# Kernel tuning notes

Measured on AMD Instinct MI355X. Metric: run time of the kernel, lower is better.

The kernel has to match this reference:

```python
import jax, jax.numpy as jnp
import numpy as np

EPS = 1e-08
BASE_CR = 0.5
MIN_CR = 0.1


def _layernorm(h, g, b, eps=1e-5):
    m = jnp.mean(h, axis=-1, keepdims=True)
    v = jnp.mean((h - m) ** 2, axis=-1, keepdims=True)
    return (h - m) * jax.lax.rsqrt(v + eps) * g + b


def _normalize(h, eps=1e-12):
    n = jnp.sqrt(jnp.sum(h * h, axis=-1, keepdims=True))
    return h / jnp.maximum(n, eps)


def _conv1d(h, w, b):
    # h: [B,S,D], w: [K,I,O] (WIO), cross-correlation, SAME padding (torch Conv1d padding=1, k=3)
    y = jax.lax.conv_general_dilated(h, w, window_strides=(1,), padding='SAME',
                                     dimension_numbers=('NWC', 'WIO', 'NWC'))
    return y + b


def setup_inputs() -> dict:
    key = jax.random.key(0)
    ks = jax.random.split(key, 8)
    V, L, D, B, S = 50257, 2048, 1024, 8, 2048
    inp = {
        'x': jax.random.randint(ks[0], (B, S), 0, V),
        'token_emb': jax.random.normal(ks[1], (V, D), jnp.float32) * 0.02,
        'pos_emb': jax.random.normal(ks[2], (L, D), jnp.float32) * 0.02,
        'conv1_w': jax.random.normal(ks[3], (3, D, D), jnp.float32) * 0.025,
        'conv1_b': jnp.zeros((D,), jnp.float32),
        'conv2_w': jax.random.normal(ks[4], (3, D, D), jnp.float32) * 0.025,
        'conv2_b': jnp.zeros((D,), jnp.float32),
        'proj_w': jax.random.normal(ks[5], (D, D), jnp.float32) * 0.03,
        'proj_b': jnp.zeros((D,), jnp.float32),
        'ph_w': jax.random.normal(ks[6], (D, D), jnp.float32) * 0.03,
        'ph_b': jnp.zeros((D,), jnp.float32),
        'ln_g': jnp.ones((D,), jnp.float32),
        'ln_b': jnp.zeros((D,), jnp.float32),
    }
    return inp


def reference(x, token_emb, pos_emb, conv1_w, conv1_b, conv2_w, conv2_b,
              proj_w, proj_b, ph_w, ph_b, ln_g, ln_b):
    B, S = x.shape
    # token + position embedding
    h = token_emb[x] + pos_emb[:S][None, :, :]                 # [B,S,D]
    # two conv1d + gelu (exact erf, matching torch F.gelu default)
    h = jax.nn.gelu(_conv1d(h, conv1_w, conv1_b), approximate=False)
    h = jax.nn.gelu(_conv1d(h, conv2_w, conv2_b), approximate=False)
    h = _layernorm(h, ln_g, ln_b)
    # dropout is identity in eval mode
    # S is a power of two -> next_power_of_two(S) == S, no padding
    x_fft = jnp.fft.fft(h, axis=1)                              # [B,S,D] complex64
    magnitude = jnp.abs(x_fft)
    thresh = 0.1 * jnp.max(magnitude, axis=1, keepdims=True)
    complexity = jnp.mean((magnitude > thresh).astype(jnp.float32), axis=(1, 2))  # [B]
    cr = jnp.clip(BASE_CR * (1.0 - complexity), MIN_CR, 1.0)
    N = jnp.clip((cr * S).astype(jnp.int32), 1, S)              # [B] kept coefficients
    # vectorized ragged masking (replaces per-sample python loop/scatter)
    mask = (jnp.arange(S)[None, :] < N[:, None]).astype(jnp.float32)   # [B,S]
    x_fft_c = x_fft * mask[:, :, None]
    x_ifft_raw = jnp.fft.ifft(x_fft_c, n=S, axis=1).real        # [B,S,D]
    proj_out = x_ifft_raw @ proj_w + proj_b
    x_ifft = _layernorm(proj_out, ln_g, ln_b)
    recon_target = proj_out                                     # same proj of same ifft
    # loss
    cos_sim = jnp.sum(_normalize(x_ifft) * _normalize(recon_target), axis=-1)
    cos_sim = jnp.clip(cos_sim, -1.0 + EPS, 1.0 - EPS)
    d = x_ifft - recon_target
    l1 = jnp.where(jnp.abs(d) < 1.0, 0.5 * d * d, jnp.abs(d) - 0.5)    # smooth_l1, beta=1
    proj_x = x_ifft @ ph_w + ph_b
    proj_t = recon_target @ ph_w + ph_b
    sem = jnp.mean((_normalize(proj_x) - _normalize(proj_t)) ** 2, axis=-1)  # [B,S]
    combined = 0.6 * jnp.mean(1.0 - cos_sim) + 0.2 * jnp.mean(l1, axis=-1) + 0.2 * sem
    loss = jnp.sum(combined * mask) / (jnp.sum(mask) + EPS)
    return (x_ifft, loss)
```

## Files before the change

### kernel.cpp

```cpp
#include <hip/hip_runtime.h>
#include <math.h>

#define S_LEN 2048
#define D_DIM 1024
#define B_BATCH 8
#define R_ROWS (B_BATCH * S_LEN)
#define BD_ROWS (B_BATCH * D_DIM)
#define PAD_ROWS 2050

typedef unsigned short u16;
typedef unsigned int u32;
typedef __attribute__((ext_vector_type(8))) short bf16x8;
typedef __attribute__((ext_vector_type(4))) float f32x4;

__device__ __forceinline__ u16 f2bf(float f) {
    u32 x = __float_as_uint(f);
    u32 r = (x + 0x7fffu + ((x >> 16) & 1u)) >> 16;
    return (u16)r;
}
__device__ __forceinline__ float bf2f(u16 u) {
    return __uint_as_float(((u32)u) << 16);
}
__device__ __forceinline__ float gelu_exact(float x) {
    return 0.5f * x * (1.0f + erff(x * 0.70710678118654752f));
}
__device__ __forceinline__ int dr4(int v) {
    v = __brev((unsigned)v) >> 22;
    return ((v & 0x155) << 1) | ((v >> 1) & 0x155);
}
#define PIDX(i) ((i) + ((i) >> 5))

#define GLDS(gsrc, ldst)                                                                   \
    __builtin_amdgcn_global_load_lds(                                                      \
        (const __attribute__((address_space(1))) u32*)(gsrc),                              \
        (__attribute__((address_space(3))) u32*)(ldst), 16, 0, 0)

#define WAIT_LGKM0 do { asm volatile("s_waitcnt lgkmcnt(0)" ::: "memory");                 \
                        __builtin_amdgcn_sched_barrier(0); } while (0)
#define WAIT_VM(n)   do { asm volatile("s_waitcnt vmcnt(" #n ")" ::: "memory");            \
                          __builtin_amdgcn_sched_barrier(0); } while (0)

__global__ __launch_bounds__(256) void zero_pads(u16* __restrict__ P0, u16* __restrict__ P1)
{
    const int bid = blockIdx.x;
    u16* P = (bid >= 16) ? P1 : P0;
    const int ridx = bid & 15;
    const int b = ridx >> 1;
    const size_t row = (size_t)b * PAD_ROWS + (size_t)(ridx & 1) * (PAD_ROWS - 1);
    ((uint2*)(P + row * D_DIM))[threadIdx.x] = make_uint2(0u, 0u);
}

__global__ __launch_bounds__(256) void wconv(const float* __restrict__ W, u16* __restrict__ WT)
{
    __shared__ float t[32][33];
    const int tap = blockIdx.z;
    const int n0 = blockIdx.x * 32, k0 = blockIdx.y * 32;
    const int tx = threadIdx.x, ty = threadIdx.y;
    const float* ip = W + (size_t)tap * D_DIM * D_DIM;
    u16* op = WT + (size_t)tap * D_DIM * D_DIM;
#pragma unroll
    for (int u = 0; u < 4; u++)
        t[ty + u * 8][tx] = ip[(size_t)(k0 + ty + u * 8) * D_DIM + n0 + tx];
    __syncthreads();
#pragma unroll
    for (int u = 0; u < 4; u++)
        op[(size_t)(n0 + ty + u * 8) * D_DIM + k0 + tx] = f2bf(t[tx][ty + u * 8]);
}

__global__ __launch_bounds__(256) void wconv_inter(
    const float* __restrict__ W, const float* __restrict__ g, u16* __restrict__ WTI)
{
    __shared__ float t[32][33];
    const int n0 = blockIdx.x * 32, k0 = blockIdx.y * 32;
    const int tx = threadIdx.x, ty = threadIdx.y;
#pragma unroll
    for (int u = 0; u < 4; u++)
        t[ty + u * 8][tx] = W[(size_t)(k0 + ty + u * 8) * D_DIM + n0 + tx];
    __syncthreads();
    const float gk = g[k0 + tx];
#pragma unroll
    for (int u = 0; u < 4; u++) {
        const int n = n0 + ty + u * 8;
        const float w = t[tx][ty + u * 8];
        WTI[((size_t)(2 * n) << 10) + k0 + tx] = f2bf(w);
        WTI[((size_t)(2 * n + 1) << 10) + k0 + tx] = f2bf(w * gk);
    }
}

__global__ __launch_bounds__(256) void gemv_ph(
    const u16* __restrict__ WTI, const float* __restrict__ lnb,
    const float* __restrict__ phb, float* __restrict__ vg, float* __restrict__ c0)
{
    const int wid = threadIdx.x >> 6, lane = threadIdx.x & 63;
    const int n = blockIdx.x * 4 + wid;
    const u16* r0 = WTI + ((size_t)(2 * n) << 10) + lane * 16;
    const u16* r1 = WTI + ((size_t)(2 * n + 1) << 10) + lane * 16;
    float sb = 0.f, sg = 0.f;
#pragma unroll
    for (int h = 0; h < 2; h++) {
        uint4 w0 = *(const uint4*)(r0 + h * 8);
        uint4 w1 = *(const uint4*)(r1 + h * 8);
        float a[8], b8[8];
        a[0] = bf2f((u16)(w0.x & 0xffff)); a[1] = bf2f((u16)(w0.x >> 16));
        a[2] = bf2f((u16)(w0.y & 0xffff)); a[3] = bf2f((u16)(w0.y >> 16));
        a[4] = bf2f((u16)(w0.z & 0xffff)); a[5] = bf2f((u16)(w0.z >> 16));
        a[6] = bf2f((u16)(w0.w & 0xffff)); a[7] = bf2f((u16)(w0.w >> 16));
        b8[0] = bf2f((u16)(w1.x & 0xffff)); b8[1] = bf2f((u16)(w1.x >> 16));
        b8[2] = bf2f((u16)(w1.y & 0xffff)); b8[3] = bf2f((u16)(w1.y >> 16));
        b8[4] = bf2f((u16)(w1.z & 0xffff)); b8[5] = bf2f((u16)(w1.z >> 16));
        b8[6] = bf2f((u16)(w1.w & 0xffff)); b8[7] = bf2f((u16)(w1.w >> 16));
        const int kb = lane * 16 + h * 8;
        float4 l0 = *(const float4*)(lnb + kb), l1 = *(const float4*)(lnb + kb + 4);
        sb += a[0]*l0.x + a[1]*l0.y + a[2]*l0.z + a[3]*l0.w
            + a[4]*l1.x + a[5]*l1.y + a[6]*l1.z + a[7]*l1.w;
        sg += b8[0] + b8[1] + b8[2] + b8[3] + b8[4] + b8[5] + b8[6] + b8[7];
    }
#pragma unroll
    for (int off = 32; off > 0; off >>= 1) {
        sg += __shfl_xor(sg, off);
        sb += __shfl_xor(sb, off);
    }
    if (lane == 0) { vg[n] = sg; c0[n] = sb + phb[n]; }
}

__global__ __launch_bounds__(256) void emb_kernel(
    const int* __restrict__ x, const float* __restrict__ tok,
    const float* __restrict__ pos, u16* __restrict__ P0)
{
    const int row = blockIdx.x;
    const int tid = threadIdx.x;
    const int t = x[row];
    const int s = row & (S_LEN - 1);
    const int b = row >> 11;
    float4 a = ((const float4*)(tok + (size_t)t * D_DIM))[tid];
    float4 p = ((const float4*)(pos + (size_t)s * D_DIM))[tid];
    uint2 v;
    v.x = (u32)f2bf(a.x + p.x) | ((u32)f2bf(a.y + p.y) << 16);
    v.y = (u32)f2bf(a.z + p.z) | ((u32)f2bf(a.w + p.w) << 16);
    ((uint2*)(P0 + ((size_t)b * PAD_ROWS + 1 + s) * D_DIM))[tid] = v;
}

__global__ __launch_bounds__(512, 2) void gemm_8ph(
    const u16* __restrict__ A, const u16* __restrict__ WT,
    const float* __restrict__ bias,
    float* __restrict__ outF, u16* __restrict__ outB,
    float* __restrict__ rowS, float* __restrict__ rowQ,
    int ntaps, int doGelu, int aPadded, int outBPadded)
{
    __shared__ u16 As[2][2][8192];
    __shared__ u16 Bs[2][2][8192];
    const int tid = threadIdx.x;
    const int wid = tid >> 6, lane = tid & 63;
    const int wm = wid >> 2, wn = wid & 3;
    const int l15 = lane & 15, l4 = lane >> 4;
    const int flat = blockIdx.y * 4 + blockIdx.x;
    const int xcd = flat & 7;
    const int ii = flat >> 3;
    const int by = xcd * 8 + (ii >> 2);
    const int bx = ii & 3;
    const int row0 = by * 256;
    const int col0 = bx * 256;
    const int b = row0 >> 11;
    const int srow0 = row0 & (S_LEN - 1);
    const int nt = ntaps * 16;
    const int NI = nt >> 1;

    const int stR = tid >> 2;
    const int stKc = (((tid & 3) ^ ((tid >> 3) & 3)) << 3);
    const int ldsOff = tid * 16;
    const int swz4 = ((l4 ^ ((l15 >> 1) & 3)) << 4);

#define STAGE_A(T_, s_) do {                                                               \
        const int tap_ = (T_) >> 4;                                                        \
        const int kb_ = ((T_) & 15) * 64 + (s_) * 32 + stKc;                               \
        const size_t ar_ = (aPadded ? (size_t)(b * PAD_ROWS + srow0 + tap_)                \
                                    : (size_t)row0);                                       \
        GLDS(A + ((ar_ + stR) << 10) + kb_,                                                \
             (char*)&As[(T_) & 1][s_][0] + ldsOff);                                        \
        GLDS(A + ((ar_ + stR + 128) << 10) + kb_,                                          \
             (char*)&As[(T_) & 1][s_][0] + ldsOff + 8192);                                 \
    } while (0)
#define STAGE_B(T_, s_) do {                                                               \
        const int tap_ = (T_) >> 4;                                                        \
        const int kb_ = ((T_) & 15) * 64 + (s_) * 32 + stKc;                               \
        const u16* wp_ = WT + ((size_t)tap_ << 20) + ((size_t)(col0 + stR) << 10) + kb_;   \
        GLDS(wp_, (char*)&Bs[(T_) & 1][s_][0] + ldsOff);                                   \
        GLDS(wp_ + (size_t)(128 << 10), (char*)&Bs[(T_) & 1][s_][0] + ldsOff + 8192);      \
    } while (0)
#define RD_A(dst_, buf_, s_, mih_) do {                                                    \
        const char* p_ = (const char*)&As[buf_][s_][0]                                     \
                         + (size_t)(wm * 128 + (mih_) * 64 + l15) * 64 + swz4;             \
        dst_[0] = *(const bf16x8*)(p_);                                                    \
        dst_[1] = *(const bf16x8*)(p_ + 1024);                                             \
        dst_[2] = *(const bf16x8*)(p_ + 2048);                                             \
        dst_[3] = *(const bf16x8*)(p_ + 3072);                                             \
    } while (0)
#define RD_B(dst_, buf_, s_) do {                                                          \
        const char* p_ = (const char*)&Bs[buf_][s_][0]                                     \
                         + (size_t)(wn * 64 + l15) * 64 + swz4;                            \
        dst_[0] = *(const bf16x8*)(p_);                                                    \
        dst_[1] = *(const bf16x8*)(p_ + 1024);                                             \
        dst_[2] = *(const bf16x8*)(p_ + 2048);                                             \
        dst_[3] = *(const bf16x8*)(p_ + 3072);                                             \
    } while (0)
#define MF(mih_, av_, bv_) do {                                                            \
        __builtin_amdgcn_s_setprio(1);                                                     \
        _Pragma("unroll")                                                                  \
        for (int mi_ = 0; mi_ < 4; mi_++)                                                  \
            _Pragma("unroll")                                                              \
            for (int ni_ = 0; ni_ < 4; ni_++)                                              \
                acc[(mih_) * 4 + mi_][ni_] = __builtin_amdgcn_mfma_f32_16x16x32_bf16(      \
                    av_[mi_], bv_[ni_], acc[(mih_) * 4 + mi_][ni_], 0, 0, 0);              \
        __builtin_amdgcn_s_setprio(0);                                                     \
    } while (0)
#define BAR __builtin_amdgcn_s_barrier()

    f32x4 acc[8][4];
#pragma unroll
    for (int m = 0; m < 8; m++)
#pragma unroll
        for (int n = 0; n < 4; n++) acc[m][n] = (f32x4){0.f, 0.f, 0.f, 0.f};

    STAGE_A(0, 0); STAGE_B(0, 0);
    STAGE_A(0, 1); STAGE_B(0, 1);
    STAGE_A(1, 0); STAGE_B(1, 0);
    WAIT_VM(4);
    BAR;

    for (int i = 0; i < NI; ++i) {
        const int o = 2 * i + 1;
        const int e2 = 2 * i + 2, o2 = 2 * i + 3;
        const bool last = (i == NI - 1);
        bf16x8 a[4], bv[4];
        RD_A(a, 0, 0, 0); RD_B(bv, 0, 0);
        STAGE_A(o, 1);
        BAR; WAIT_LGKM0;
        MF(0, a, bv);
        BAR;
        RD_A(a, 0, 0, 1);
        STAGE_B(o, 1);
        BAR; WAIT_LGKM0;
        MF(1, a, bv);
        BAR;
        RD_A(a, 0, 1, 0); RD_B(bv, 0, 1);
        if (!last) STAGE_A(e2, 0);
        BAR; WAIT_LGKM0;
        MF(0, a, bv);
        BAR;
        RD_A(a, 0, 1, 1);
        if (!last) STAGE_B(e2, 0);
        BAR; WAIT_LGKM0;
        MF(1, a, bv);
        if (last) { WAIT_VM(0); } else { WAIT_VM(4); }
        BAR;
        RD_A(a, 1, 0, 0); RD_B(bv, 1, 0);
        if (!last) STAGE_A(e2, 1);
        BAR; WAIT_LGKM0;
        MF(0, a, bv);
        BAR;
        RD_A(a, 1, 0, 1);
        if (!last) STAGE_B(e2, 1);
        BAR; WAIT_LGKM0;
        MF(1, a, bv);
        BAR;
        RD_A(a, 1, 1, 0); RD_B(bv, 1, 1);
        if (!last) STAGE_A(o2, 0);
        BAR; WAIT_LGKM0;
        MF(0, a, bv);
        BAR;
        RD_A(a, 1, 1, 1);
        if (!last) STAGE_B(o2, 0);
        BAR; WAIT_LGKM0;
        MF(1, a, bv);
        if (!last) { WAIT_VM(4); }
        BAR;
    }
#undef STAGE_A

    float bb[4];
#pragma unroll
    for (int ni = 0; ni < 4; ni++) bb[ni] = bias[col0 + wn * 64 + ni * 16 + l15];

#pragma unroll
    for (int mi = 0; mi < 8; mi++) {
#pragma unroll
        for (int reg = 0; reg < 4; reg++) {
            const int row = row0 + wm * 128 + mi * 16 + l4 * 4 + reg;
            float s_ = 0.f, q_ = 0.f;
#pragma unroll
            for (int ni = 0; ni < 4; ni++) {
                const int col = col0 + wn * 64 + ni * 16 + l15;
                float v = acc[mi][ni][reg] + bb[ni];
                if (doGelu) v = gelu_exact(v);
                if (outF) outF[(size_t)row * D_DIM + col] = v;
                if (outB) {
                    const size_t orow = outBPadded
                        ? ((size_t)(row >> 11) * PAD_ROWS + 1 + (size_t)(row & (S_LEN - 1)))
                        : (size_t)row;
                    outB[orow * D_DIM + col] = f2bf(v);
                }
                if (rowS) { s_ += v; q_ = fmaf(v, v, q_); }
            }
            if (rowS) {
#pragma unroll
                for (int off = 1; off < 16; off <<= 1) {
                    s_ += __shfl_xor(s_, off);
                    q_ += __shfl_xor(q_, off);
                }
                if (l15 == 0) {
                    atomicAdd(&rowS[row], s_);
                    atomicAdd(&rowQ[row], q_);
                }
            }
        }
    }
}

__global__ __launch_bounds__(512, 2) void phstats_8ph(
    const u16* __restrict__ A, const u16* __restrict__ WTI,
    const float* __restrict__ phb, const float* __restrict__ vg,
    const float* __restrict__ c0,
    const float* __restrict__ rowS2, const float* __restrict__ rowQ2,
    const int* __restrict__ Ndev,
    float* __restrict__ Sxx, float* __restrict__ Stt, float* __restrict__ Sxt)
{
    __shared__ u16 As[2][2][8192];
    __shared__ u16 Bs[2][2][8192];
    const int tid = threadIdx.x;
    const int wid = tid >> 6, lane = tid & 63;
    const int wm = wid >> 2, wn = wid & 3;
    const int l15 = lane & 15, l4 = lane >> 4;
    const int flat = blockIdx.y * 8 + blockIdx.x;
    const int xcd = flat & 7;
    const int ii = flat >> 3;
    const int by = xcd * 4 + (ii >> 3);
    const int bx = ii & 7;
    const int batch = by >> 2;
    const int rb = by & 3;
    if (rb * 256 >= Ndev[batch]) return;
    const int row0 = batch * S_LEN + rb * 256;
    const int col0 = bx * 256;
    const int NI = 8;

    const int stR = tid >> 2;
    const int stKc = (((tid & 3) ^ ((tid >> 3) & 3)) << 3);
    const int ldsOff = tid * 16;
    const int swz4 = ((l4 ^ ((l15 >> 1) & 3)) << 4);

#define STAGE_A(T_, s_) do {                                                               \
        const int kb_ = ((T_) & 15) * 64 + (s_) * 32 + stKc;                               \
        GLDS(A + (((size_t)row0 + stR) << 10) + kb_,                                       \
             (char*)&As[(T_) & 1][s_][0] + ldsOff);                                        \
        GLDS(A + (((size_t)row0 + stR + 128) << 10) + kb_,                                 \
             (char*)&As[(T_) & 1][s_][0] + ldsOff + 8192);                                 \
    } while (0)
#define STAGE_BI(T_, s_) do {                                                              \
        const int kb_ = ((T_) & 15) * 64 + (s_) * 32 + stKc;                               \
        const u16* wp_ = WTI + ((size_t)(col0 + stR) << 10) + kb_;                         \
        GLDS(wp_, (char*)&Bs[(T_) & 1][s_][0] + ldsOff);                                   \
        GLDS(wp_ + (size_t)(128 << 10), (char*)&Bs[(T_) & 1][s_][0] + ldsOff + 8192);      \
    } while (0)

    f32x4 acc[8][4];
#pragma unroll
    for (int m = 0; m < 8; m++)
#pragma unroll
        for (int n = 0; n < 4; n++) acc[m][n] = (f32x4){0.f, 0.f, 0.f, 0.f};

    STAGE_A(0, 0); STAGE_BI(0, 0);
    STAGE_A(0, 1); STAGE_BI(0, 1);
    STAGE_A(1, 0); STAGE_BI(1, 0);
    WAIT_VM(4);
    BAR;

    for (int i = 0; i < NI; ++i) {
        const int o = 2 * i + 1;
        const int e2 = 2 * i + 2, o2 = 2 * i + 3;
        const bool last = (i == NI - 1);
        bf16x8 a[4], bv[4];
        RD_A(a, 0, 0, 0); RD_B(bv, 0, 0);
        STAGE_A(o, 1);
        BAR; WAIT_LGKM0;
        MF(0, a, bv);
        BAR;
        RD_A(a, 0, 0, 1);
        STAGE_BI(o, 1);
        BAR; WAIT_LGKM0;
        MF(1, a, bv);
        BAR;
        RD_A(a, 0, 1, 0); RD_B(bv, 0, 1);
        if (!last) STAGE_A(e2, 0);
        BAR; WAIT_LGKM0;
        MF(0, a, bv);
        BAR;
        RD_A(a, 0, 1, 1);
        if (!last) STAGE_BI(e2, 0);
        BAR; WAIT_LGKM0;
        MF(1, a, bv);
        if (last) { WAIT_VM(0); } else { WAIT_VM(4); }
        BAR;
        RD_A(a, 1, 0, 0); RD_B(bv, 1, 0);
        if (!last) STAGE_A(e2, 1);
        BAR; WAIT_LGKM0;
        MF(0, a, bv);
        BAR;
        RD_A(a, 1, 0, 1);
        if (!last) STAGE_BI(e2, 1);
        BAR; WAIT_LGKM0;
        MF(1, a, bv);
        BAR;
        RD_A(a, 1, 1, 0); RD_B(bv, 1, 1);
        if (!last) STAGE_A(o2, 0);
        BAR; WAIT_LGKM0;
        MF(0, a, bv);
        BAR;
        RD_A(a, 1, 1, 1);
        if (!last) STAGE_BI(o2, 0);
        BAR; WAIT_LGKM0;
        MF(1, a, bv);
        if (!last) { WAIT_VM(4); }
        BAR;
    }
#undef STAGE_A
#undef STAGE_BI
#undef RD_A
#undef RD_B
#undef MF
#undef BAR

    float phv[4], vgv[4], c0v[4];
#pragma unroll
    for (int ni = 0; ni < 4; ni++) {
        const int col = col0 + wn * 64 + ni * 16 + l15;
        const int j = col >> 1;
        phv[ni] = phb[j]; vgv[ni] = vg[j]; c0v[ni] = c0[j];
    }
    const bool odd = (l15 & 1) != 0;
#pragma unroll
    for (int mi = 0; mi < 8; mi++) {
#pragma unroll
        for (int reg = 0; reg < 4; reg++) {
            const int row = row0 + wm * 128 + mi * 16 + l4 * 4 + reg;
            const float mS = rowS2[row] * (1.0f / D_DIM);
            const float var = rowQ2[row] * (1.0f / D_DIM) - mS * mS;
            const float rsv = rsqrtf(var + 1e-5f);
            const float mrs = mS * rsv;
            float sxx = 0.f, stt = 0.f, sxt = 0.f;
#pragma unroll
            for (int ni = 0; ni < 4; ni++) {
                const float raw = acc[mi][ni][reg];
                const float val = odd ? (rsv * raw - mrs * vgv[ni] + c0v[ni])
                                      : (raw + phv[ni]);
                const float par = __shfl_xor(val, 1);
                const float pt = odd ? par : val;
                const float px = odd ? val : par;
                stt = fmaf(pt, pt, stt);
                sxx = fmaf(px, px, sxx);
                sxt = fmaf(pt, px, sxt);
            }
#pragma unroll
            for (int off = 1; off < 16; off <<= 1) {
                sxx += __shfl_xor(sxx, off);
                stt += __shfl_xor(stt, off);
                sxt += __shfl_xor(sxt, off);
            }
            if (l15 == 0) {
                atomicAdd(&Sxx[row], 0.5f * sxx);
                atomicAdd(&Stt[row], 0.5f * stt);
                atomicAdd(&Sxt[row], 0.5f * sxt);
            }
        }
    }
}

__global__ __launch_bounds__(256) void transposeLN(
    const u16* __restrict__ in, const float* __restrict__ rowS,
    const float* __restrict__ rowQ,
    const float* __restrict__ g, const float* __restrict__ beta,
    float* __restrict__ out)
{
    __shared__ float t[32][33];
    const int b = blockIdx.z;
    const int n0 = blockIdx.x * 32, m0 = blockIdx.y * 32;
    const int tx = threadIdx.x, ty = threadIdx.y;
    const u16* ip = in + (size_t)b * S_LEN * D_DIM;
    float* op = out + (size_t)b * S_LEN * D_DIM;
#pragma unroll
    for (int u = 0; u < 4; u++)
        t[ty + u * 8][tx] = bf2f(ip[(size_t)(m0 + ty + u * 8) * D_DIM + n0 + tx]);
    __syncthreads();
    const int row = b * S_LEN + m0 + tx;
    const float mS = rowS[row] * (1.0f / D_DIM);
    const float var = rowQ[row] * (1.0f / D_DIM) - mS * mS;
    const float rs = rsqrtf(var + 1e-5f);
#pragma unroll
    for (int u = 0; u < 4; u++) {
        const int d = n0 + ty + u * 8;
        const float val = (t[tx][ty + u * 8] - mS) * rs * g[d] + beta[d];
        op[(size_t)d * S_LEN + m0 + tx] = val;
    }
}

__global__ __launch_bounds__(256) void fft_fwd(
    const float* __restrict__ in, u32* __restrict__ X, int* __restrict__ counts)
{
    __shared__ float re[1056], im[1056], twr[1024], twi[1024];
    __shared__ float redf[4];
    __shared__ int redi[4];
    const int tid = threadIdx.x;
    const int row = blockIdx.x;
    const float2* src = (const float2*)(in + (size_t)row * S_LEN);
#pragma unroll
    for (int u = 0; u < 4; u++) {
        int e = tid + u * 256;
        float ang = -3.14159265358979f * (float)e * (1.0f / 512.0f);
        float sn, cs; __sincosf(ang, &sn, &cs);
        twr[e] = cs; twi[e] = sn;
    }
#pragma unroll
    for (int u = 0; u < 4; u++) {
        int t = tid + u * 256;
        float2 z = src[t];
        int p = PIDX(dr4(t));
        re[p] = z.x; im[p] = z.y;
    }
    __syncthreads();
#pragma unroll
    for (int s = 1; s <= 5; ++s) {
        const int mq = 1 << (2 * (s - 1));
        const int fsh = 2 * (5 - s);
        const int j = tid & (mq - 1);
        const int g = tid >> (2 * (s - 1));
        const int i0 = (g << (2 * s)) + j;
        const int e1 = j << fsh;
        const int p0 = PIDX(i0), p1 = PIDX(i0 + mq), p2 = PIDX(i0 + 2 * mq), p3 = PIDX(i0 + 3 * mq);
        float a0r = re[p0], a0i = im[p0];
        float a1r = re[p1], a1i = im[p1];
        float a2r = re[p2], a2i = im[p2];
        float a3r = re[p3], a3i = im[p3];
        float w1r = twr[e1], w1i = twi[e1];
        float w2r = twr[2 * e1], w2i = twi[2 * e1];
        float w3r = twr[3 * e1], w3i = twi[3 * e1];
        float b1r = a1r * w1r - a1i * w1i, b1i = a1r * w1i + a1i * w1r;
        float b2r = a2r * w2r - a2i * w2i, b2i = a2r * w2i + a2i * w2r;
        float b3r = a3r * w3r - a3i * w3i, b3i = a3r * w3i + a3i * w3r;
        float t0r = a0r + b2r, t0i = a0i + b2i;
        float t1r = a0r - b2r, t1i = a0i - b2i;
        float t2r = b1r + b3r, t2i = b1i + b3i;
        float t3r = b1r - b3r, t3i = b1i - b3i;
        re[p0] = t0r + t2r; im[p0] = t0i + t2i;
        re[p2] = t0r - t2r; im[p2] = t0i - t2i;
        re[p1] = t1r + t3i; im[p1] = t1i - t3r;
        re[p3] = t1r - t3i; im[p3] = t1i + t3r;
        __syncthreads();
    }
    u32* dst = X + (size_t)row * 1024;
    float mag[4];
    float xtra = 0.0f;
    float lmax = 0.0f;
#pragma unroll
    for (int u = 0; u < 4; u++) {
        int k = tid + u * 256;
        int mk = (1024 - k) & 1023;
        float rk = re[PIDX(k)], ik = im[PIDX(k)];
        float rm = re[PIDX(mk)], imm = im[PIDX(mk)];
        float er = 0.5f * (rk + rm);
        float ei = 0.5f * (ik - imm);
        float orr = 0.5f * (ik + imm);
        float oii = -0.5f * (rk - rm);
        float ang = -3.14159265358979f * (float)k * (1.0f / 1024.0f);
        float sn, cs; __sincosf(ang, &sn, &cs);
        float xr = er + orr * cs - oii * sn;
        float xi = ei + orr * sn + oii * cs;
        dst[k] = (u32)f2bf(xr) | ((u32)f2bf(xi) << 16);
        float m2 = xr * xr + xi * xi;
        mag[u] = m2;
        lmax = fmaxf(lmax, m2);
        if (k == 0) {
            float x1024 = re[PIDX(0)] - im[PIDX(0)];
            xtra = x1024 * x1024;
            lmax = fmaxf(lmax, xtra);
        }
    }
#pragma unroll
    for (int off = 32; off > 0; off >>= 1) lmax = fmaxf(lmax, __shfl_xor(lmax, off));
    if ((tid & 63) == 0) redf[tid >> 6] = lmax;
    __syncthreads();
    const float bmax = fmaxf(fmaxf(redf[0], redf[1]), fmaxf(redf[2], redf[3]));
    const float thr = 0.01f * bmax;
    int lc = 0;
#pragma unroll
    for (int u = 0; u < 4; u++) {
        int k = tid + u * 256;
        lc += (mag[u] > thr) ? ((k == 0) ? 1 : 2) : 0;
    }
    if (tid == 0) lc += (xtra > thr) ? 1 : 0;
#pragma unroll
    for (int off = 32; off > 0; off >>= 1) lc += __shfl_xor(lc, off);
    if ((tid & 63) == 0) redi[tid >> 6] = lc;
    __syncthreads();
    if (tid == 0)
        atomicAdd(&counts[(row >> 10) * 64 + (row & 63)],
                  redi[0] + redi[1] + redi[2] + redi[3]);
}

__global__ void calc_n(const int* __restrict__ counts, int* __restrict__ Ndev)
{
// ... 191 lines not shown
        rowA[row] = 1.0f - cs;
        rowL1[row] = l1;
    }
}

__global__ __launch_bounds__(1024) void final_loss(
    const float* __restrict__ rowA, const float* __restrict__ rowL1,
    const float* __restrict__ Sxx, const float* __restrict__ Stt,
    const float* __restrict__ Sxt,
    const int* __restrict__ Ndev, float* __restrict__ out)
{
    const int tid = threadIdx.x;
    float sa = 0.f, sb = 0.f;
#pragma unroll
    for (int i = 0; i < 16; i++) {
        int r = tid + i * 1024;
        sa += rowA[r];
        int b = r >> 11, s = r & (S_LEN - 1);
        if (s < Ndev[b]) {
            float sx = Sxx[r], st = Stt[r], sxtv = Sxt[r];
            float nxx = fmaxf(sqrtf(sx), 1e-12f);
            float ntt = fmaxf(sqrtf(st), 1e-12f);
            float sem = (sx / (nxx * nxx) + st / (ntt * ntt)
                         - 2.0f * sxtv / (nxx * ntt)) * (1.0f / D_DIM);
            sb += 0.2f * (rowL1[r] * (1.0f / D_DIM)) + 0.2f * sem;
        }
    }
#pragma unroll
    for (int off = 32; off > 0; off >>= 1) {
        sa += __shfl_xor(sa, off);
        sb += __shfl_xor(sb, off);
    }
    __shared__ float ra[16], rb[16];
    if ((tid & 63) == 0) { ra[tid >> 6] = sa; rb[tid >> 6] = sb; }
    __syncthreads();
    if (tid == 0) {
        float A = 0.f, Bs = 0.f;
#pragma unroll
        for (int i = 0; i < 16; i++) { A += ra[i]; Bs += rb[i]; }
        int K = 0;
        for (int b = 0; b < B_BATCH; b++) K += Ndev[b];
        float Kf = (float)K;
        float M = A * (1.0f / 16384.0f);
        out[(size_t)R_ROWS * D_DIM] = (0.6f * M * Kf + Bs) / (Kf + 1e-8f);
    }
}

extern "C" void kernel_launch(void* const* d_in, const int* in_sizes, int n_in,
                              void* d_out, int out_size, void* d_ws, size_t ws_size,
                              hipStream_t stream)
{
    (void)in_sizes; (void)n_in; (void)out_size; (void)ws_size;
    const int*   x       = (const int*)  d_in[0];
    const float* tok     = (const float*)d_in[1];
    const float* pos     = (const float*)d_in[2];
    const float* conv1_w = (const float*)d_in[3];
    const float* conv1_b = (const float*)d_in[4];
    const float* conv2_w = (const float*)d_in[5];
    const float* conv2_b = (const float*)d_in[6];
    const float* proj_w  = (const float*)d_in[7];
    const float* proj_b  = (const float*)d_in[8];
    const float* ph_w    = (const float*)d_in[9];
    const float* ph_b    = (const float*)d_in[10];
    const float* ln_g    = (const float*)d_in[11];
    const float* ln_b    = (const float*)d_in[12];
    float* out = (float*)d_out;

    char* ws = (char*)d_ws;
    int*    counts = (int*)(ws);
    int*    Ndev   = (int*)(ws + 2048);
    float*  Sxx    = (float*)(ws + 266240);
    float*  Stt    = (float*)(ws + 331776);
    float*  Sxt    = (float*)(ws + 397312);
    float*  rowA   = (float*)(ws + 462848);
    float*  rowL1  = (float*)(ws + 528384);
    float*  vg     = (float*)(ws + 593920);
    float*  c0     = (float*)(ws + 598016);
    float*  rowS   = (float*)(ws + 602112);
    float*  rowQ   = (float*)(ws + 667648);
    float*  rowS2  = (float*)(ws + 733184);
    float*  rowQ2  = (float*)(ws + 798720);
    const size_t MB = 1ull << 20;
    u16*   WT   = (u16*)(ws + 1 * MB);
    u16*   WTI  = WT;
    u16*   P0   = (u16*)(ws + 17 * MB);
    u16*   P1   = (u16*)(ws + 50 * MB);
    u32*   Xs   = (u32*)(ws + 83 * MB);
    float* F32B = (float*)(ws + 148 * MB);

    hipMemsetAsync(ws, 0, MB, stream);
    zero_pads<<<32, 256, 0, stream>>>(P0, P1);
    wconv<<<dim3(32, 32, 3), dim3(32, 8), 0, stream>>>(conv1_w, WT);
    wconv<<<dim3(32, 32, 3), dim3(32, 8), 0, stream>>>(conv2_w, WT + 3u * (1u << 20));
    wconv<<<dim3(32, 32, 1), dim3(32, 8), 0, stream>>>(proj_w, WT + 6u * (1u << 20));
    emb_kernel<<<R_ROWS, 256, 0, stream>>>(x, tok, pos, P0);
    gemm_8ph<<<dim3(4, 64), 512, 0, stream>>>(P0, WT, conv1_b,
                                              nullptr, P1, nullptr, nullptr, 3, 1, 1, 1);
    wconv_inter<<<dim3(32, 32, 1), dim3(32, 8), 0, stream>>>(ph_w, ln_g, WTI);
    gemv_ph<<<256, 256, 0, stream>>>(WTI, ln_b, ph_b, vg, c0);
    gemm_8ph<<<dim3(4, 64), 512, 0, stream>>>(P1, WT + 3u * (1u << 20), conv2_b,
                                              nullptr, P0, rowS, rowQ, 3, 1, 1, 0);
    transposeLN<<<dim3(32, 64, 8), dim3(32, 8), 0, stream>>>(P0, rowS, rowQ,
                                                             ln_g, ln_b, F32B);
    fft_fwd<<<BD_ROWS, 256, 0, stream>>>(F32B, Xs, counts);
    calc_n<<<1, 64, 0, stream>>>(counts, Ndev);
    fft_inv<<<BD_ROWS, 256, 0, stream>>>(Xs, Ndev, P1);
    transpose_bb<<<dim3(64, 32, 8), dim3(32, 8), 0, stream>>>(P1, P0, D_DIM, S_LEN);
    gemm_8ph<<<dim3(4, 64), 512, 0, stream>>>(P0, WT + 6u * (1u << 20), proj_b,
                                              nullptr, P1, rowS2, rowQ2, 1, 0, 0, 0);
    ln_loss<<<R_ROWS, 256, 0, stream>>>(P1, ln_g, ln_b, out, rowS2, rowQ2, rowA, rowL1);
    phstats_8ph<<<dim3(8, 32), 512, 0, stream>>>(P1, WTI, ph_b, vg, c0,
                                                 rowS2, rowQ2, Ndev, Sxx, Stt, Sxt);
    final_loss<<<1, 1024, 0, stream>>>(rowA, rowL1, Sxx, Stt, Sxt, Ndev, out);
}
```

Baseline: 537.3 us.

## Add dedicated conv GEMM kernel, merge weight prep, store LN transpose as bf16

The two conv layers now run in a new gemm_c2 kernel. It uses 256x128 tiles, a three-buffer LDS pipeline and four blocks per CU, in place of the generic 256x256 gemm_8ph with two blocks per CU. The four weight-conversion launches are merged into one wprep kernel, and the ph GEMV is moved earlier. The transposed LayerNorm output feeding the FFT is stored as packed bf16 instead of fp32, which halves that intermediate's traffic. The bf16 FFT input costs some precision, and the smaller conv tiles reload the A operand more often.

```diff
diff --git a/kernel.cpp b/kernel.cpp
--- a/kernel.cpp
+++ b/kernel.cpp
@@ -50,40 +50,39 @@
     ((uint2*)(P + row * D_DIM))[threadIdx.x] = make_uint2(0u, 0u);
 }
 
-__global__ __launch_bounds__(256) void wconv(const float* __restrict__ W, u16* __restrict__ WT)
+__global__ __launch_bounds__(256) void wprep(
+    const float* __restrict__ c1, const float* __restrict__ c2,
+    const float* __restrict__ pj, const float* __restrict__ ph,
+    const float* __restrict__ g, u16* __restrict__ WT)
 {
     __shared__ float t[32][33];
-    const int tap = blockIdx.z;
+    const int z = blockIdx.z;
     const int n0 = blockIdx.x * 32, k0 = blockIdx.y * 32;
     const int tx = threadIdx.x, ty = threadIdx.y;
-    const float* ip = W + (size_t)tap * D_DIM * D_DIM;
-    u16* op = WT + (size_t)tap * D_DIM * D_DIM;
+    const float* src;
+    if (z < 3)      src = c1 + (size_t)z * D_DIM * D_DIM;
+    else if (z < 6) src = c2 + (size_t)(z - 3) * D_DIM * D_DIM;
+    else if (z == 6) src = pj;
+    else            src = ph;
 #pragma unroll
     for (int u = 0; u < 4; u++)
-        t[ty + u * 8][tx] = ip[(size_t)(k0 + ty + u * 8) * D_DIM + n0 + tx];
+        t[ty + u * 8][tx] = src[(size_t)(k0 + ty + u * 8) * D_DIM + n0 + tx];
     __syncthreads();
-#pragma unroll
-    for (int u = 0; u < 4; u++)
-        op[(size_t)(n0 + ty + u * 8) * D_DIM + k0 + tx] = f2bf(t[tx][ty + u * 8]);
-}
-
-__global__ __launch_bounds__(256) void wconv_inter(
-    const float* __restrict__ W, const float* __restrict__ g, u16* __restrict__ WTI)
-{
-    __shared__ float t[32][33];
-    const int n0 = blockIdx.x * 32, k0 = blockIdx.y * 32;
-    const int tx = threadIdx.x, ty = threadIdx.y;
-#pragma unroll
-    for (int u = 0; u < 4; u++)
-        t[ty + u * 8][tx] = W[(size_t)(k0 + ty + u * 8) * D_DIM + n0 + tx];
-    __syncthreads();
-    const float gk = g[k0 + tx];
-#pragma unroll
-    for (int u = 0; u < 4; u++) {
-        const int n = n0 + ty + u * 8;
-        const float w = t[tx][ty + u * 8];
-        WTI[((size_t)(2 * n) << 10) + k0 + tx] = f2bf(w);
-        WTI[((size_t)(2 * n + 1) << 10) + k0 + tx] = f2bf(w * gk);
+    if (z < 7) {
+        u16* op = WT + (size_t)z * D_DIM * D_DIM;
+#pragma unroll
+        for (int u = 0; u < 4; u++)
+            op[(size_t)(n0 + ty + u * 8) * D_DIM + k0 + tx] = f2bf(t[tx][ty + u * 8]);
+    } else {
+        u16* WTI = WT + 7u * (1u << 20);
+        const float gk = g[k0 + tx];
+#pragma unroll
+        for (int u = 0; u < 4; u++) {
+            const int n = n0 + ty + u * 8;
+            const float w = t[tx][ty + u * 8];
+            WTI[((size_t)(2 * n) << 10) + k0 + tx] = f2bf(w);
+            WTI[((size_t)(2 * n + 1) << 10) + k0 + tx] = f2bf(w * gk);
+        }
     }
 }
 
@@ -140,12 +139,146 @@
     ((uint2*)(P0 + ((size_t)b * PAD_ROWS + 1 + s) * D_DIM))[tid] = v;
 }
 
+__global__ __launch_bounds__(512, 4) void gemm_c2(
+    const u16* __restrict__ A, const u16* __restrict__ WT,
+    const float* __restrict__ bias, u16* __restrict__ outB,
+    float* __restrict__ rowS, float* __restrict__ rowQ,
+    int outBPadded)
+{
+    __shared__ u16 As[3][8192];
+    __shared__ u16 Bs[3][4096];
+    const int tid = threadIdx.x;
+    const int wid = tid >> 6, lane = tid & 63;
+    const int wm = wid >> 1, wn = wid & 1;
+    const int l15 = lane & 15, l4 = lane >> 4;
+    const int flat = blockIdx.y * 8 + blockIdx.x;
+    const int xcd = flat & 7;
+    const int ii = flat >> 3;
+    const int by = xcd * 8 + (ii >> 3);
+    const int bx = ii & 7;
+    const int row0 = by * 256;
+    const int col0 = bx * 128;
+    const int b = row0 >> 11;
+    const int srow0 = row0 & (S_LEN - 1);
+    const int nt = 96;
+
+    const int stR = tid >> 2;
+    const int stKc = (((tid & 3) ^ ((tid >> 3) & 3)) << 3);
+    const int ldsOff = tid * 16;
+    const int swz4 = ((l4 ^ ((l15 >> 1) & 3)) << 4);
+
+#define C2_SA(T_, B_) do {                                                                 \
+        const int tap_ = (T_) >> 5;                                                        \
+        const int kb_ = ((T_) & 31) * 32 + stKc;                                           \
+        const size_t ar_ = (size_t)(b * PAD_ROWS + srow0 + tap_);                          \
+        GLDS(A + ((ar_ + stR) << 10) + kb_, (char*)&As[B_][0] + ldsOff);                   \
+        GLDS(A + ((ar_ + stR + 128) << 10) + kb_, (char*)&As[B_][0] + ldsOff + 8192);      \
+    } while (0)
+#define C2_SB(T_, B_) do {                                                                 \
+        const int tap_ = (T_) >> 5;                                                        \
+        const int kb_ = ((T_) & 31) * 32 + stKc;                                           \
+        GLDS(WT + ((size_t)tap_ << 20) + ((size_t)(col0 + stR) << 10) + kb_,               \
+             (char*)&Bs[B_][0] + ldsOff);                                                  \
+    } while (0)
+#define C2_RA(B_) do {                                                                     \
+        const char* p_ = (const char*)&As[B_][0] + (size_t)(wm * 64 + l15) * 64 + swz4;    \
+        a[0] = *(const bf16x8*)(p_);                                                       \
+        a[1] = *(const bf16x8*)(p_ + 1024);                                                \
+        a[2] = *(const bf16x8*)(p_ + 2048);                                                \
+        a[3] = *(const bf16x8*)(p_ + 3072);                                                \
+    } while (0)
+#define C2_RB(B_) do {                                                                     \
+        const char* p_ = (const char*)&Bs[B_][0] + (size_t)(wn * 64 + l15) * 64 + swz4;    \
+        bv[0] = *(const bf16x8*)(p_);                                                      \
+        bv[1] = *(const bf16x8*)(p_ + 1024);                                               \
+        bv[2] = *(const bf16x8*)(p_ + 2048);                                               \
+        bv[3] = *(const bf16x8*)(p_ + 3072);                                               \
+    } while (0)
+#define C2_MF do {                                                                         \
+        __builtin_amdgcn_s_setprio(1);                                                     \
+        _Pragma("unroll")                                                                  \
+        for (int mi_ = 0; mi_ < 4; mi_++)                                                  \
+            _Pragma("unroll")                                                              \
+            for (int ni_ = 0; ni_ < 4; ni_++)                                              \
+                acc[mi_][ni_] = __builtin_amdgcn_mfma_f32_16x16x32_bf16(                   \
+                    a[mi_], bv[ni_], acc[mi_][ni_], 0, 0, 0);                              \
+        __builtin_amdgcn_s_setprio(0);                                                     \
+    } while (0)
+#define C2_BAR __builtin_amdgcn_s_barrier()
+#define C2_SUB(TT_, RB_, SB_) do {                                                         \
+        C2_RA(RB_); C2_RB(RB_);                                                            \
+        if ((TT_) + 2 < nt) { C2_SA((TT_) + 2, SB_); C2_SB((TT_) + 2, SB_); }              \
+        C2_BAR; WAIT_LGKM0;                                                                \
+        C2_MF;                                                                             \
+        if ((TT_) + 2 < nt) { WAIT_VM(3); } else { WAIT_VM(0); }                           \
+        C2_BAR;                                                                            \
+    } while (0)
+
+    f32x4 acc[4][4];
+#pragma unroll
+    for (int m = 0; m < 4; m++)
+#pragma unroll
+        for (int n = 0; n < 4; n++) acc[m][n] = (f32x4){0.f, 0.f, 0.f, 0.f};
+
+    bf16x8 a[4], bv[4];
+    C2_SA(0, 0); C2_SB(0, 0);
+    C2_SA(1, 1); C2_SB(1, 1);
+    WAIT_VM(3);
+    C2_BAR;
+
+    for (int t = 0; t < nt; t += 3) {
+        C2_SUB(t,     0, 2);
+        C2_SUB(t + 1, 1, 0);
+        C2_SUB(t + 2, 2, 1);
+    }
+#undef C2_SA
+#undef C2_SB
+#undef C2_RA
+#undef C2_RB
+#undef C2_MF
+#undef C2_BAR
+#undef C2_SUB
+
+    float bb[4];
+#pragma unroll
+    for (int ni = 0; ni < 4; ni++) bb[ni] = bias[col0 + wn * 64 + ni * 16 + l15];
+
+#pragma unroll
+    for (int mi = 0; mi < 4; mi++) {
+#pragma unroll
+        for (int reg = 0; reg < 4; reg++) {
+            const int row = row0 + wm * 64 + mi * 16 + l4 * 4 + reg;
+            float s_ = 0.f, q_ = 0.f;
+#pragma unroll
+            for (int ni = 0; ni < 4; ni++) {
+                const int col = col0 + wn * 64 + ni * 16 + l15;
+                float v = gelu_exact(acc[mi][ni][reg] + bb[ni]);
+                const size_t orow = outBPadded
+                    ? ((size_t)(row >> 11) * PAD_ROWS + 1 + (size_t)(row & (S_LEN - 1)))
+                    : (size_t)row;
+                outB[orow * D_DIM + col] = f2bf(v);
+                if (rowS) { s_ += v; q_ = fmaf(v, v, q_); }
+            }
+            if (rowS) {
+#pragma unroll
+                for (int off = 1; off < 16; off <<= 1) {
+                    s_ += __shfl_xor(s_, off);
+                    q_ += __shfl_xor(q_, off);
+                }
+                if (l15 == 0) {
+                    atomicAdd(&rowS[row], s_);
+                    atomicAdd(&rowQ[row], q_);
+                }
+            }
+        }
+    }
+}
+
 __global__ __launch_bounds__(512, 2) void gemm_8ph(
     const u16* __restrict__ A, const u16* __restrict__ WT,
     const float* __restrict__ bias,
-    float* __restrict__ outF, u16* __restrict__ outB,
-    float* __restrict__ rowS, float* __restrict__ rowQ,
-    int ntaps, int doGelu, int aPadded, int outBPadded)
+    u16* __restrict__ outB,
+    float* __restrict__ rowS, float* __restrict__ rowQ)
 {
     __shared__ u16 As[2][2][8192];
     __shared__ u16 Bs[2][2][8192];
@@ -160,10 +293,7 @@
     const int bx = ii & 3;
     const int row0 = by * 256;
     const int col0 = bx * 256;
-    const int b = row0 >> 11;
-    const int srow0 = row0 & (S_LEN - 1);
-    const int nt = ntaps * 16;
-    const int NI = nt >> 1;
+    const int NI = 8;
 
     const int stR = tid >> 2;
     const int stKc = (((tid & 3) ^ ((tid >> 3) & 3)) << 3);
@@ -171,19 +301,15 @@
     const int swz4 = ((l4 ^ ((l15 >> 1) & 3)) << 4);
 
 #define STAGE_A(T_, s_) do {                                                               \
-        const int tap_ = (T_) >> 4;                                                        \
         const int kb_ = ((T_) & 15) * 64 + (s_) * 32 + stKc;                               \
-        const size_t ar_ = (aPadded ? (size_t)(b * PAD_ROWS + srow0 + tap_)                \
-                                    : (size_t)row0);                                       \
-        GLDS(A + ((ar_ + stR) << 10) + kb_,                                                \
+        GLDS(A + (((size_t)row0 + stR) << 10) + kb_,                                       \
              (char*)&As[(T_) & 1][s_][0] + ldsOff);                                        \
-        GLDS(A + ((ar_ + stR + 128) << 10) + kb_,                                          \
+        GLDS(A + (((size_t)row0 + stR + 128) << 10) + kb_,                                 \
              (char*)&As[(T_) & 1][s_][0] + ldsOff + 8192);                                 \
     } while (0)
 #define STAGE_B(T_, s_) do {                                                               \
-        const int tap_ = (T_) >> 4;                                                        \
         const int kb_ = ((T_) & 15) * 64 + (s_) * 32 + stKc;                               \
-        const u16* wp_ = WT + ((size_t)tap_ << 20) + ((size_t)(col0 + stR) << 10) + kb_;   \
+        const u16* wp_ = WT + ((size_t)(col0 + stR) << 10) + kb_;                          \
         GLDS(wp_, (char*)&Bs[(T_) & 1][s_][0] + ldsOff);                                   \
         GLDS(wp_ + (size_t)(128 << 10), (char*)&Bs[(T_) & 1][s_][0] + ldsOff + 8192);      \
     } while (0)
@@ -214,6 +340,55 @@
         __builtin_amdgcn_s_setprio(0);                                                     \
     } while (0)
 #define BAR __builtin_amdgcn_s_barrier()
+#define LOOP8PH                                                                            \
+    for (int i = 0; i < NI; ++i) {                                                         \
+        const int o = 2 * i + 1;                                                           \
+        const int e2 = 2 * i + 2, o2 = 2 * i + 3;                                          \
+        const bool last = (i == NI - 1);                                                   \
+        bf16x8 a[4], bv[4];                                                                \
+        RD_A(a, 0, 0, 0); RD_B(bv, 0, 0);                                                  \
+        STAGE_A(o, 1);                                                                     \
+        BAR; WAIT_LGKM0;                                                                   \
+        MF(0, a, bv);                                                                      \
+        BAR;                                                                               \
+        RD_A(a, 0, 0, 1);                                                                  \
+        STAGE_B(o, 1);                                                                     \
+        BAR; WAIT_LGKM0;                                                                   \
+        MF(1, a, bv);                                                                      \
+        BAR;                                                                               \
+        RD_A(a, 0, 1, 0); RD_B(bv, 0, 1);                                                  \
+        if (!last) STAGE_A(e2, 0);                                                         \
+        BAR; WAIT_LGKM0;                                                                   \
+        MF(0, a, bv);                                                                      \
+        BAR;                                                                               \
+        RD_A(a, 0, 1, 1);                                                                  \
+        if (!last) STAGE_B(e2, 0);                                                         \
+        BAR; WAIT_LGKM0;                                                                   \
+        MF(1, a, bv);                                                                      \
+        if (last) { WAIT_VM(0); } else { WAIT_VM(4); }                                     \
+        BAR;                                                                               \
+        RD_A(a, 1, 0, 0); RD_B(bv, 1, 0);                                                  \
+        if (!last) STAGE_A(e2, 1);                                                         \
+        BAR; WAIT_LGKM0;                                                                   \
+        MF(0, a, bv);                                                                      \
+        BAR;                                                                               \
+        RD_A(a, 1, 0, 1);                                                                  \
+        if (!last) STAGE_B(e2, 1);                                                         \
+        BAR; WAIT_LGKM0;                                                                   \
+        MF(1, a, bv);                                                                      \
+        BAR;                                                                               \
+        RD_A(a, 1, 1, 0); RD_B(bv, 1, 1);                                                  \
+        if (!last) STAGE_A(o2, 0);                                                         \
+        BAR; WAIT_LGKM0;                                                                   \
+        MF(0, a, bv);                                                                      \
+        BAR;                                                                               \
+        RD_A(a, 1, 1, 1);                                                                  \
+        if (!last) STAGE_B(o2, 0);                                                         \
+        BAR; WAIT_LGKM0;                                                                   \
+        MF(1, a, bv);                                                                      \
+        if (!last) { WAIT_VM(4); }                                                         \
+        BAR;                                                                               \
+    }
 
     f32x4 acc[8][4];
 #pragma unroll
@@ -226,56 +401,7 @@
     STAGE_A(1, 0); STAGE_B(1, 0);
     WAIT_VM(4);
     BAR;
-
-    for (int i = 0; i < NI; ++i) {
-        const int o = 2 * i + 1;
-        const int e2 = 2 * i + 2, o2 = 2 * i + 3;
-        const bool last = (i == NI - 1);
-        bf16x8 a[4], bv[4];
-        RD_A(a, 0, 0, 0); RD_B(bv, 0, 0);
-        STAGE_A(o, 1);
-        BAR; WAIT_LGKM0;
-        MF(0, a, bv);
-        BAR;
-        RD_A(a, 0, 0, 1);
-        STAGE_B(o, 1);
-        BAR; WAIT_LGKM0;
-        MF(1, a, bv);
-        BAR;
-        RD_A(a, 0, 1, 0); RD_B(bv, 0, 1);
-        if (!last) STAGE_A(e2, 0);
-        BAR; WAIT_LGKM0;
-        MF(0, a, bv);
-        BAR;
-        RD_A(a, 0, 1, 1);
-        if (!last) STAGE_B(e2, 0);
-        BAR; WAIT_LGKM0;
-        MF(1, a, bv);
-        if (last) { WAIT_VM(0); } else { WAIT_VM(4); }
-        BAR;
-        RD_A(a, 1, 0, 0); RD_B(bv, 1, 0);
-        if (!last) STAGE_A(e2, 1);
-        BAR; WAIT_LGKM0;
-        MF(0, a, bv);
-        BAR;
-        RD_A(a, 1, 0, 1);
-        if (!last) STAGE_B(e2, 1);
-        BAR; WAIT_LGKM0;
-        MF(1, a, bv);
-        BAR;
-        RD_A(a, 1, 1, 0); RD_B(bv, 1, 1);
-        if (!last) STAGE_A(o2, 0);
-        BAR; WAIT_LGKM0;
-        MF(0, a, bv);
-        BAR;
-        RD_A(a, 1, 1, 1);
-        if (!last) STAGE_B(o2, 0);
-        BAR; WAIT_LGKM0;
-        MF(1, a, bv);
-        if (!last) { WAIT_VM(4); }
-        BAR;
-    }
-#undef STAGE_A
+    LOOP8PH
 
     float bb[4];
 #pragma unroll
@@ -291,33 +417,24 @@
             for (int ni = 0; ni < 4; ni++) {
                 const int col = col0 + wn * 64 + ni * 16 + l15;
                 float v = acc[mi][ni][reg] + bb[ni];
-                if (doGelu) v = gelu_exact(v);
-                if (outF) outF[(size_t)row * D_DIM + col] = v;
-                if (outB) {
-                    const size_t orow = outBPadded
-                        ? ((size_t)(row >> 11) * PAD_ROWS + 1 + (size_t)(row & (S_LEN - 1)))
-                        : (size_t)row;
-                    outB[orow * D_DIM + col] = f2bf(v);
-                }
-                if (rowS) { s_ += v; q_ = fmaf(v, v, q_); }
+                outB[(size_t)row * D_DIM + col] = f2bf(v);
+                s_ += v; q_ = fmaf(v, v, q_);
             }
-            if (rowS) {
-#pragma unroll
-                for (int off = 1; off < 16; off <<= 1) {
-                    s_ += __shfl_xor(s_, off);
-                    q_ += __shfl_xor(q_, off);
-                }
-                if (l15 == 0) {
-                    atomicAdd(&rowS[row], s_);
-                    atomicAdd(&rowQ[row], q_);
-                }
+#pragma unroll
+            for (int off = 1; off < 16; off <<= 1) {
+                s_ += __shfl_xor(s_, off);
+                q_ += __shfl_xor(q_, off);
+            }
+            if (l15 == 0) {
+                atomicAdd(&rowS[row], s_);
+                atomicAdd(&rowQ[row], q_);
             }
         }
     }
 }
 
 __global__ __launch_bounds__(512, 2) void phstats_8ph(
-    const u16* __restrict__ A, const u16* __restrict__ WTI,
+    const u16* __restrict__ A, const u16* __restrict__ WT,
     const float* __restrict__ phb, const float* __restrict__ vg,
     const float* __restrict__ c0,
     const float* __restrict__ rowS2, const float* __restrict__ rowQ2,
@@ -347,86 +464,25 @@
     const int ldsOff = tid * 16;
     const int swz4 = ((l4 ^ ((l15 >> 1) & 3)) << 4);
 
-#define STAGE_A(T_, s_) do {                                                               \
-        const int kb_ = ((T_) & 15) * 64 + (s_) * 32 + stKc;                               \
-        GLDS(A + (((size_t)row0 + stR) << 10) + kb_,                                       \
-             (char*)&As[(T_) & 1][s_][0] + ldsOff);                                        \
-        GLDS(A + (((size_t)row0 + stR + 128) << 10) + kb_,                                 \
-             (char*)&As[(T_) & 1][s_][0] + ldsOff + 8192);                                 \
-    } while (0)
-#define STAGE_BI(T_, s_) do {                                                              \
-        const int kb_ = ((T_) & 15) * 64 + (s_) * 32 + stKc;                               \
-        const u16* wp_ = WTI + ((size_t)(col0 + stR) << 10) + kb_;                         \
-        GLDS(wp_, (char*)&Bs[(T_) & 1][s_][0] + ldsOff);                                   \
-        GLDS(wp_ + (size_t)(128 << 10), (char*)&Bs[(T_) & 1][s_][0] + ldsOff + 8192);      \
-    } while (0)
-
     f32x4 acc[8][4];
 #pragma unroll
     for (int m = 0; m < 8; m++)
 #pragma unroll
         for (int n = 0; n < 4; n++) acc[m][n] = (f32x4){0.f, 0.f, 0.f, 0.f};
 
-    STAGE_A(0, 0); STAGE_BI(0, 0);
-    STAGE_A(0, 1); STAGE_BI(0, 1);
-    STAGE_A(1, 0); STAGE_BI(1, 0);
+    STAGE_A(0, 0); STAGE_B(0, 0);
+    STAGE_A(0, 1); STAGE_B(0, 1);
+    STAGE_A(1, 0); STAGE_B(1, 0);
     WAIT_VM(4);
     BAR;
-
-    for (int i = 0; i < NI; ++i) {
-        const int o = 2 * i + 1;
-        const int e2 = 2 * i + 2, o2 = 2 * i + 3;
-        const bool last = (i == NI - 1);
-        bf16x8 a[4], bv[4];
-        RD_A(a, 0, 0, 0); RD_B(bv, 0, 0);
-        STAGE_A(o, 1);
-        BAR; WAIT_LGKM0;
-        MF(0, a, bv);
-        BAR;
-        RD_A(a, 0, 0, 1);
-        STAGE_BI(o, 1);
-        BAR; WAIT_LGKM0;
-        MF(1, a, bv);
-        BAR;
-        RD_A(a, 0, 1, 0); RD_B(bv, 0, 1);
-        if (!last) STAGE_A(e2, 0);
-        BAR; WAIT_LGKM0;
-        MF(0, a, bv);
-        BAR;
-        RD_A(a, 0, 1, 1);
-        if (!last) STAGE_BI(e2, 0);
-        BAR; WAIT_LGKM0;
-        MF(1, a, bv);
-        if (last) { WAIT_VM(0); } else { WAIT_VM(4); }
-        BAR;
-        RD_A(a, 1, 0, 0); RD_B(bv, 1, 0);
-        if (!last) STAGE_A(e2, 1);
-        BAR; WAIT_LGKM0;
-        MF(0, a, bv);
-        BAR;
-        RD_A(a, 1, 0, 1);
-        if (!last) STAGE_BI(e2, 1);
-        BAR; WAIT_LGKM0;
-        MF(1, a, bv);
-        BAR;
-        RD_A(a, 1, 1, 0); RD_B(bv, 1, 1);
-        if (!last) STAGE_A(o2, 0);
-        BAR; WAIT_LGKM0;
-        MF(0, a, bv);
-        BAR;
-        RD_A(a, 1, 1, 1);
-        if (!last) STAGE_BI(o2, 0);
-        BAR; WAIT_LGKM0;
-        MF(1, a, bv);
-        if (!last) { WAIT_VM(4); }
-        BAR;
-    }
+    LOOP8PH
 #undef STAGE_A
-#undef STAGE_BI
+#undef STAGE_B
 #undef RD_A
 #undef RD_B
 #undef MF
 #undef BAR
+#undef LOOP8PH
 
     float phv[4], vgv[4], c0v[4];
 #pragma unroll
@@ -477,14 +533,14 @@
     const u16* __restrict__ in, const float* __restrict__ rowS,
     const float* __restrict__ rowQ,
     const float* __restrict__ g, const float* __restrict__ beta,
-    float* __restrict__ out)
+    u16* __restrict__ out)
 {
     __shared__ float t[32][33];
     const int b = blockIdx.z;
     const int n0 = blockIdx.x * 32, m0 = blockIdx.y * 32;
     const int tx = threadIdx.x, ty = threadIdx.y;
     const u16* ip = in + (size_t)b * S_LEN * D_DIM;
-    float* op = out + (size_t)b * S_LEN * D_DIM;
+    u16* op = out + (size_t)b * S_LEN * D_DIM;
 #pragma unroll
     for (int u = 0; u < 4; u++)
         t[ty + u * 8][tx] = bf2f(ip[(size_t)(m0 + ty + u * 8) * D_DIM + n0 + tx]);
@@ -497,19 +553,19 @@
     for (int u = 0; u < 4; u++) {
         const int d = n0 + ty + u * 8;
         const float val = (t[tx][ty + u * 8] - mS) * rs * g[d] + beta[d];
-        op[(size_t)d * S_LEN + m0 + tx] = val;
+        op[(size_t)d * S_LEN + m0 + tx] = f2bf(val);
     }
 }
 
 __global__ __launch_bounds__(256) void fft_fwd(
-    const float* __restrict__ in, u32* __restrict__ X, int* __restrict__ counts)
+    const u16* __restrict__ in, u32* __restrict__ X, int* __restrict__ counts)
 {
     __shared__ float re[1056], im[1056], twr[1024], twi[1024];
     __shared__ float redf[4];
     __shared__ int redi[4];
     const int tid = threadIdx.x;
     const int row = blockIdx.x;
-    const float2* src = (const float2*)(in + (size_t)row * S_LEN);
+    const u32* src = (const u32*)(in + (size_t)row * S_LEN);
 #pragma unroll
     for (int u = 0; u < 4; u++) {
         int e = tid + u * 256;
@@ -520,9 +576,9 @@
 #pragma unroll
     for (int u = 0; u < 4; u++) {
         int t = tid + u * 256;
-        float2 z = src[t];
+        u32 w = src[t];
         int p = PIDX(dr4(t));
-        re[p] = z.x; im[p] = z.y;
+        re[p] = bf2f((u16)(w & 0xffff)); im[p] = bf2f((u16)(w >> 16));
     }
     __syncthreads();
 #pragma unroll
@@ -880,32 +936,30 @@
     float*  rowQ2  = (float*)(ws + 798720);
     const size_t MB = 1ull << 20;
     u16*   WT   = (u16*)(ws + 1 * MB);
-    u16*   WTI  = WT;
-    u16*   P0   = (u16*)(ws + 17 * MB);
-    u16*   P1   = (u16*)(ws + 50 * MB);
-    u32*   Xs   = (u32*)(ws + 83 * MB);
-    float* F32B = (float*)(ws + 148 * MB);
+    u16*   WTI  = WT + 7u * (1u << 20);
+    u16*   P0   = (u16*)(ws + 19 * MB);
+    u16*   P1   = (u16*)(ws + 52 * MB);
+    u32*   Xs   = (u32*)(ws + 85 * MB);
+    u16*   BTR  = (u16*)(ws + 118 * MB);
 
     hipMemsetAsync(ws, 0, MB, stream);
     zero_pads<<<32, 256, 0, stream>>>(P0, P1);
-    wconv<<<dim3(32, 32, 3), dim3(32, 8), 0, stream>>>(conv1_w, WT);
-    wconv<<<dim3(32, 32, 3), dim3(32, 8), 0, stream>>>(conv2_w, WT + 3u * (1u << 20));
-    wconv<<<dim3(32, 32, 1), dim3(32, 8), 0, stream>>>(proj_w, WT + 6u * (1u << 20));
+    wprep<<<dim3(32, 32, 8), dim3(32, 8), 0, stream>>>(conv1_w, conv2_w, proj_w,
+                                                       ph_w, ln_g, WT);
+    gemv_ph<<<256, 256, 0, stream>>>(WTI, ln_b, ph_b, vg, c0);
     emb_kernel<<<R_ROWS, 256, 0, stream>>>(x, tok, pos, P0);
-    gemm_8ph<<<dim3(4, 64), 512, 0, stream>>>(P0, WT, conv1_b,
-                                              nullptr, P1, nullptr, nullptr, 3, 1, 1, 1);
-    wconv_inter<<<dim3(32, 32, 1), dim3(32, 8), 0, stream>>>(ph_w, ln_g, WTI);
-    gemv_ph<<<256, 256, 0, stream>>>(WTI, ln_b, ph_b, vg, c0);
-    gemm_8ph<<<dim3(4, 64), 512, 0, stream>>>(P1, WT + 3u * (1u << 20), conv2_b,
-                                              nullptr, P0, rowS, rowQ, 3, 1, 1, 0);
+    gemm_c2<<<dim3(8, 64), 512, 0, stream>>>(P0, WT, conv1_b, P1,
+                                             nullptr, nullptr, 1);
+    gemm_c2<<<dim3(8, 64), 512, 0, stream>>>(P1, WT + 3u * (1u << 20), conv2_b, P0,
+                                             rowS, rowQ, 0);
     transposeLN<<<dim3(32, 64, 8), dim3(32, 8), 0, stream>>>(P0, rowS, rowQ,
-                                                             ln_g, ln_b, F32B);
-    fft_fwd<<<BD_ROWS, 256, 0, stream>>>(F32B, Xs, counts);
+                                                             ln_g, ln_b, BTR);
+    fft_fwd<<<BD_ROWS, 256, 0, stream>>>(BTR, Xs, counts);
     calc_n<<<1, 64, 0, stream>>>(counts, Ndev);
     fft_inv<<<BD_ROWS, 256, 0, stream>>>(Xs, Ndev, P1);
     transpose_bb<<<dim3(64, 32, 8), dim3(32, 8), 0, stream>>>(P1, P0, D_DIM, S_LEN);
     gemm_8ph<<<dim3(4, 64), 512, 0, stream>>>(P0, WT + 6u * (1u << 20), proj_b,
-                                              nullptr, P1, rowS2, rowQ2, 1, 0, 0, 0);
+                                              P1, rowS2, rowQ2);
     ln_loss<<<R_ROWS, 256, 0, stream>>>(P1, ln_g, ln_b, out, rowS2, rowQ2, rowA, rowL1);
     phstats_8ph<<<dim3(8, 32), 512, 0, stream>>>(P1, WTI, ph_b, vg, c0,
                                                  rowS2, rowQ2, Ndev, Sxx, Stt, Sxt);
```

Result: slower. 558.8 us (+4.0%).
